# Kernel optimization log

Hardware: AMD Instinct MI355X
Metric: run time of the kernel (lower is better)

The kernel has to match this reference:

```python
import jax, jax.numpy as jnp
import numpy as np

ALPHA = 0.2  # leaky_relu negative slope
N = 100000
E = 3200000

def _gat_layer(h_in, edge, W, a):
    # h = x @ W ; score_e = leaky_relu([h_src || h_dst] @ a) computed without
    # materializing the [E, 2d] concat: a = [a_src; a_dst]
    h = h_in @ W                                  # [N, d]
    d = W.shape[1]
    s_src = h @ a[:d, 0]                          # [N]
    s_dst = h @ a[d:, 0]                          # [N]
    src, dst = edge[0], edge[1]
    score = jax.nn.leaky_relu(s_src[src] + s_dst[dst], negative_slope=ALPHA)  # [E]
    # sparse softmax over dim=1: normalize per source row (edge[0])
    m = jax.ops.segment_max(score, src, num_segments=N)      # [N], -inf for empty rows (never gathered)
    e = jnp.exp(score - m[src])                               # [E]
    z = jax.ops.segment_sum(e, src, num_segments=N)           # [N]
    attn = e / z[src]                                         # [E]
    # output[i] = sum_{(i,j) in E} attn_ij * h[j]; empty rows -> 0 (matches to_dense @ h)
    out = jax.ops.segment_sum(attn[:, None] * h[dst], src, num_segments=N)  # [N, d]
    return jax.nn.elu(out)

def setup_inputs() -> dict:
    key = jax.random.key(0)
    ks = jax.random.split(key, 8)
    return {
        "x": jax.random.normal(ks[0], (N, 256), dtype=jnp.float32),
        "edge": jax.random.randint(ks[1], (2, E), 0, N, dtype=jnp.int64) if jax.config.jax_enable_x64 else jax.random.randint(ks[1], (2, E), 0, N, dtype=jnp.int32),
        "W0": jax.random.normal(ks[2], (256, 256), dtype=jnp.float32) * 0.06,
        "a0": jax.random.normal(ks[3], (512, 1), dtype=jnp.float32) * 0.06,
        "W1": jax.random.normal(ks[4], (256, 128), dtype=jnp.float32) * 0.07,
        "a1": jax.random.normal(ks[5], (256, 1), dtype=jnp.float32) * 0.08,
        "lin_w": jax.random.normal(ks[6], (128, 40), dtype=jnp.float32) * 0.09,
        "lin_b": jax.random.normal(ks[7], (40,), dtype=jnp.float32) * 0.01,
    }

def reference(x, edge, W0, a0, W1, a1, lin_w, lin_b):
    # inference mode: dropout is identity
    h0 = _gat_layer(x, edge, W0, a0)    # [N, 256]
    h1 = _gat_layer(h0, edge, W1, a1)   # [N, 128]
    logits = h1 @ lin_w + lin_b         # [N, 40]
    return jax.nn.log_softmax(logits, axis=1)
```

## Files before the change

### kernel.cpp

```cpp
#include <hip/hip_runtime.h>
#include <cstddef>
#include <cstdint>

#define LRELU_ALPHA 0.2f
#define BIN_SHIFT 9
#define BIN_ROWS  (1 << BIN_SHIFT)
#define DST_BITS 17
#define DST_MASK ((1 << DST_BITS) - 1)

typedef _Float16 f16x8 __attribute__((ext_vector_type(8)));
typedef _Float16 f16x4 __attribute__((ext_vector_type(4)));
typedef _Float16 f16x2 __attribute__((ext_vector_type(2)));
typedef float    f32x4 __attribute__((ext_vector_type(4)));

__global__ __launch_bounds__(256) void bucket_count_kernel(const int* __restrict__ src,
                                                           int* __restrict__ bhist, int E)
{
    __shared__ int hist[256];
    int t = threadIdx.x;
    hist[t] = 0;
    __syncthreads();
    int base = blockIdx.x * 4096;
#pragma unroll
    for (int j = 0; j < 16; ++j) {
        int i = base + j * 256 + t;
        if (i < E) atomicAdd(&hist[src[i] >> BIN_SHIFT], 1);
    }
    __syncthreads();
    if (hist[t]) atomicAdd(&bhist[t], hist[t]);
}

__global__ __launch_bounds__(256) void bucket_scan_kernel(const int* __restrict__ bhist,
                                                          int* __restrict__ bbase,
                                                          int* __restrict__ gcur, int E)
{
    __shared__ int buf[256];
    int t = threadIdx.x;
    int v = bhist[t];
    buf[t] = v;
    __syncthreads();
    for (int off = 1; off < 256; off <<= 1) {
        int u = (t >= off) ? buf[t - off] : 0;
        __syncthreads();
        buf[t] += u;
        __syncthreads();
    }
    int excl = buf[t] - v;
    bbase[t] = excl;
    gcur[t] = excl;
    if (t == 255) bbase[256] = buf[255];
}

__global__ __launch_bounds__(256) void pass1_bin_kernel(const int* __restrict__ src,
                                                        const int* __restrict__ dst,
                                                        int* __restrict__ gcur,
                                                        int* __restrict__ pairs, int E)
{
    __shared__ int hist[256];
    __shared__ int cur[256];
    int t = threadIdx.x;
    hist[t] = 0;
    __syncthreads();
    int base = blockIdx.x * 4096;
    int s_[16], d_[16];
#pragma unroll
    for (int j = 0; j < 16; ++j) {
        int i = base + j * 256 + t;
        if (i < E) {
            s_[j] = src[i];
            d_[j] = dst[i];
            atomicAdd(&hist[s_[j] >> BIN_SHIFT], 1);
        } else s_[j] = -1;
    }
    __syncthreads();
    cur[t] = atomicAdd(&gcur[t], hist[t]);
    __syncthreads();
#pragma unroll
    for (int j = 0; j < 16; ++j) {
        if (s_[j] >= 0) {
            int pos = atomicAdd(&cur[s_[j] >> BIN_SHIFT], 1);
            pairs[pos] = ((s_[j] & (BIN_ROWS - 1)) << DST_BITS) | d_[j];
        }
    }
}

__global__ __launch_bounds__(256) void row_count_kernel(const int* __restrict__ pairs,
                                                        const int* __restrict__ bbase,
                                                        int* __restrict__ cnt, int N)
{
    __shared__ int c[BIN_ROWS];
    int b = blockIdx.x, t = threadIdx.x;
    int rowbase = b << BIN_SHIFT;
    int nrows = min(BIN_ROWS, N - rowbase);
    c[t] = 0; c[t + 256] = 0;
    __syncthreads();
    int beg = bbase[b], end = bbase[b + 1];
    for (int i = beg + t; i < end; i += 256)
        atomicAdd(&c[pairs[i] >> DST_BITS], 1);
    __syncthreads();
    if (t < nrows) cnt[rowbase + t] = c[t];
    if (t + 256 < nrows) cnt[rowbase + t + 256] = c[t + 256];
}

__global__ __launch_bounds__(256) void bsum_kernel(const int* __restrict__ cnt,
                                                   int* __restrict__ bsum, int n)
{
    __shared__ int red[4];
    int b = blockIdx.x, t = threadIdx.x;
    int base = b * 1024;
    int s = 0;
#pragma unroll
    for (int j = 0; j < 4; ++j) {
        int i = base + j * 256 + t;
        s += (i < n) ? cnt[i] : 0;
    }
#pragma unroll
    for (int off = 32; off; off >>= 1) s += __shfl_xor(s, off);
    if ((t & 63) == 0) red[t >> 6] = s;
    __syncthreads();
    if (t == 0) bsum[b] = red[0] + red[1] + red[2] + red[3];
}

__global__ __launch_bounds__(128) void bscan_kernel(int* __restrict__ bsum, int nb,
                                                    int* __restrict__ rowptr, int N)
{
    __shared__ int buf[128];
    int t = threadIdx.x;
    int v = (t < nb) ? bsum[t] : 0;
    buf[t] = v;
    __syncthreads();
    for (int off = 1; off < 128; off <<= 1) {
        int u = (t >= off) ? buf[t - off] : 0;
        __syncthreads();
        buf[t] += u;
        __syncthreads();
    }
    if (t < nb) bsum[t] = buf[t] - v;
    if (t == 127) rowptr[N] = buf[127];
}

__global__ __launch_bounds__(256) void chunkscan_kernel(const int* __restrict__ cnt,
                                                        const int* __restrict__ bsum,
                                                        int* __restrict__ rowptr, int n)
{
    __shared__ int tsum[256];
    int b = blockIdx.x, t = threadIdx.x;
    int base = b * 1024 + t * 4;
    int c[4];
    int s = 0;
#pragma unroll
    for (int j = 0; j < 4; ++j) {
        int i = base + j;
        c[j] = (i < n) ? cnt[i] : 0;
        s += c[j];
    }
    tsum[t] = s;
    __syncthreads();
    for (int off = 1; off < 256; off <<= 1) {
        int u = (t >= off) ? tsum[t - off] : 0;
        __syncthreads();
        tsum[t] += u;
        __syncthreads();
    }
    int run = bsum[b] + tsum[t] - s;
#pragma unroll
    for (int j = 0; j < 4; ++j) {
        int i = base + j;
        if (i < n) { rowptr[i] = run; run += c[j]; }
    }
}

__global__ __launch_bounds__(256) void pass2_scatter_kernel(const int* __restrict__ pairs,
                                                            const int* __restrict__ bbase,
                                                            const int* __restrict__ rowptr,
                                                            int* __restrict__ csr_dst, int N)
{
    __shared__ int cur[BIN_ROWS];
    int b = blockIdx.x, t = threadIdx.x;
    int rowbase = b << BIN_SHIFT;
    int nrows = min(BIN_ROWS, N - rowbase);
    if (t < nrows) cur[t] = rowptr[rowbase + t];
    if (t + 256 < nrows) cur[t + 256] = rowptr[rowbase + t + 256];
    __syncthreads();
    int beg = bbase[b], end = bbase[b + 1];
    for (int i = beg + t; i < end; i += 256) {
        int p = pairs[i];
        int pos = atomicAdd(&cur[p >> DST_BITS], 1);
        csr_dst[pos] = p & DST_MASK;
    }
}

__global__ __launch_bounds__(256) void transpose16_kernel(const float* __restrict__ W,
                                                          _Float16* __restrict__ Wt,
                                                          int K, int Nw)
{
    int i = blockIdx.x * 256 + threadIdx.x;
    if (i < K * Nw) {
        int n = i / K, k = i - n * K;
        Wt[i] = (_Float16)W[(size_t)k * Nw + n];
    }
}

#define GBM 64
#define GBK 32
#define LDP 40

template <bool CVTA, bool FUSE_S, int GBN>
__global__ __launch_bounds__(256) void gemm16_kernel(const void* __restrict__ Ap,
                                                     const _Float16* __restrict__ Bt,
                                                     _Float16* __restrict__ C,
                                                     int M, int K,
                                                     const float* __restrict__ avec,
                                                     int aoff,
                                                     float* __restrict__ ssrc,
                                                     float* __restrict__ sdst)
{
    constexpr int NT = GBN / 64;
    __shared__ __align__(16) _Float16 Ash[GBM * LDP];
    __shared__ __align__(16) _Float16 Bsh[GBN * LDP];
    const int tid = threadIdx.x;
    const int lane = tid & 63;
    const int w = tid >> 6;
    const int m0 = blockIdx.x * GBM;
    const int l15 = lane & 15;
    const int kq = lane >> 4;
    const int sr = tid >> 2;
    const int sc = tid & 3;
    const int wc = w * (GBN / 4);

    f32x4 acc[4][NT] = {};

    for (int k0 = 0; k0 < K; k0 += GBK) {
        {
            int gm = m0 + sr;
            f16x8 v = {};
            if (gm < M) {
                if constexpr (CVTA) {
                    const float* Af = (const float*)Ap;
                    float4 u0 = *(const float4*)(Af + (size_t)gm * K + k0 + sc * 8);
                    float4 u1 = *(const float4*)(Af + (size_t)gm * K + k0 + sc * 8 + 4);
                    v[0] = (_Float16)u0.x; v[1] = (_Float16)u0.y;
                    v[2] = (_Float16)u0.z; v[3] = (_Float16)u0.w;
                    v[4] = (_Float16)u1.x; v[5] = (_Float16)u1.y;
                    v[6] = (_Float16)u1.z; v[7] = (_Float16)u1.w;
                } else {
                    v = *(const f16x8*)((const _Float16*)Ap + (size_t)gm * K + k0 + sc * 8);
                }
            }
            *(f16x8*)&Ash[sr * LDP + sc * 8] = v;
        }
#pragma unroll
        for (int it = 0; it < GBN / 64; ++it) {
            int r = sr + it * 64;
            f16x8 v = *(const f16x8*)(Bt + (size_t)r * K + k0 + sc * 8);
            *(f16x8*)&Bsh[r * LDP + sc * 8] = v;
        }
        __syncthreads();

        f16x8 af[4], bf[NT];
#pragma unroll
        for (int mt = 0; mt < 4; ++mt)
            af[mt] = *(const f16x8*)&Ash[(mt * 16 + l15) * LDP + kq * 8];
#pragma unroll
        for (int nt = 0; nt < NT; ++nt)
            bf[nt] = *(const f16x8*)&Bsh[(wc + nt * 16 + l15) * LDP + kq * 8];
#pragma unroll
        for (int mt = 0; mt < 4; ++mt)
#pragma unroll
            for (int nt = 0; nt < NT; ++nt)
                acc[mt][nt] = __builtin_amdgcn_mfma_f32_16x16x32_f16(af[mt], bf[nt],
                                                                     acc[mt][nt], 0, 0, 0);
        __syncthreads();
    }

#pragma unroll
    for (int mt = 0; mt < 4; ++mt) {
#pragma unroll
        for (int r = 0; r < 4; ++r) {
            int gm = m0 + mt * 16 + kq * 4 + r;
            if (gm < M) {
#pragma unroll
                for (int nt = 0; nt < NT; ++nt)
                    C[(size_t)gm * GBN + wc + nt * 16 + l15] = (_Float16)acc[mt][nt][r];
            }
        }
    }

    if constexpr (FUSE_S) {
        float as[NT], ad[NT];
#pragma unroll
        for (int nt = 0; nt < NT; ++nt) {
            int c = wc + nt * 16 + l15;
            as[nt] = avec[c];
            ad[nt] = avec[aoff + c];
        }
#pragma unroll
        for (int mt = 0; mt < 4; ++mt) {
#pragma unroll
            for (int r = 0; r < 4; ++r) {
                float ps = 0.f, pd = 0.f;
#pragma unroll
                for (int nt = 0; nt < NT; ++nt) {
                    float v = acc[mt][nt][r];
                    ps += v * as[nt];
                    pd += v * ad[nt];
                }
#pragma unroll
                for (int off = 1; off < 16; off <<= 1) {
                    ps += __shfl_xor(ps, off);
                    pd += __shfl_xor(pd, off);
                }
                int gm = m0 + mt * 16 + kq * 4 + r;
                if (l15 == 0 && gm < M) {
                    atomicAdd(&ssrc[gm], ps);
                    atomicAdd(&sdst[gm], pd);
                }
            }
        }
    }
}

__device__ __forceinline__ float eluf(float x) { return x > 0.f ? x : expm1f(x); }

union h2u { f16x2 h; unsigned u; };
__device__ __forceinline__ unsigned pkadd(unsigned a, unsigned b)
{
    h2u x, y; x.u = a; y.u = b; x.h += y.h; return x.u;
}

template <int D>
__global__ __launch_bounds__(256) void attnagg_kernel(const _Float16* __restrict__ h,
                                                      const float* __restrict__ ssrc,
                                                      const float* __restrict__ sdst,
                                                      const int* __restrict__ csr_dst,
                                                      const int* __restrict__ rowptr,
                                                      float* __restrict__ attn_spill,
                                                      _Float16* __restrict__ out, int nrows)
{
    constexpr int HPL = D / 16;
    constexpr int NV = HPL / 8;
    __shared__ float2 wdbuf[4][128];
    int lane = threadIdx.x & 63;
    int wv = threadIdx.x >> 6;
    int row = blockIdx.x * 4 + wv;
    if (row >= nrows) return;
    int beg = rowptr[row], end = rowptr[row + 1];
    int deg = end - beg;
    bool small = (deg <= 128);

    if (deg > 0) {
        float ss = ssrc[row];
        if (small) {
            int e0 = beg + lane, e1 = e0 + 64;
            int d0 = 0, d1 = 0;
            float sc0 = -INFINITY, sc1 = -INFINITY;
            if (e0 < end) {
                d0 = csr_dst[e0];
                float sc = ss + sdst[d0];
                sc0 = (sc > 0.f) ? sc : LRELU_ALPHA * sc;
            }
            if (e1 < end) {
                d1 = csr_dst[e1];
                float sc = ss + sdst[d1];
                sc1 = (sc > 0.f) ? sc : LRELU_ALPHA * sc;
            }
            float m = fmaxf(sc0, sc1);
#pragma unroll
            for (int off = 32; off; off >>= 1) m = fmaxf(m, __shfl_xor(m, off));
            float ex0 = (e0 < end) ? expf(sc0 - m) : 0.f;
            float ex1 = (e1 < end) ? expf(sc1 - m) : 0.f;
            float z = ex0 + ex1;
#pragma unroll
            for (int off = 32; off; off >>= 1) z += __shfl_xor(z, off);
            float rz = 1.f / z;
            if (e0 < end) wdbuf[wv][lane] = make_float2(ex0 * rz, __int_as_float(d0));
            if (e1 < end) wdbuf[wv][64 + lane] = make_float2(ex1 * rz, __int_as_float(d1));
        } else {
            float m = -INFINITY;
            for (int e = beg + lane; e < end; e += 64) {
                float sc = ss + sdst[csr_dst[e]];
                sc = (sc > 0.f) ? sc : LRELU_ALPHA * sc;
                attn_spill[e] = sc;
                m = fmaxf(m, sc);
            }
#pragma unroll
            for (int off = 32; off; off >>= 1) m = fmaxf(m, __shfl_xor(m, off));
            float z = 0.f;
            for (int e = beg + lane; e < end; e += 64) {
                float ex = expf(attn_spill[e] - m);
                attn_spill[e] = ex;
                z += ex;
            }
#pragma unroll
            for (int off = 32; off; off >>= 1) z += __shfl_xor(z, off);
            float rz = 1.f / z;
            for (int e = beg + lane; e < end; e += 64) attn_spill[e] *= rz;
        }
    }

    int sub = lane >> 4;
    int cl = lane & 15;
    const _Float16* hbase = h + cl * HPL;
    f16x8 acc[NV] = {};

    if (small) {
        int k = sub;
        for (; k + 12 < deg; k += 16) {
            float2 wd0 = wdbuf[wv][k];
            float2 wd1 = wdbuf[wv][k + 4];
            float2 wd2 = wdbuf[wv][k + 8];
            float2 wd3 = wdbuf[wv][k + 12];
            const _Float16* p0 = hbase + ((unsigned)__float_as_int(wd0.y) * D);
            const _Float16* p1 = hbase + ((unsigned)__float_as_int(wd1.y) * D);
            const _Float16* p2 = hbase + ((unsigned)__float_as_int(wd2.y) * D);
            const _Float16* p3 = hbase + ((unsigned)__float_as_int(wd3.y) * D);
            f16x8 v0[NV], v1[NV], v2[NV], v3[NV];
#pragma unroll
            for (int q = 0; q < NV; ++q) v0[q] = *(const f16x8*)(p0 + q * 8);
#pragma unroll
            for (int q = 0; q < NV; ++q) v1[q] = *(const f16x8*)(p1 + q * 8);
#pragma unroll
            for (int q = 0; q < NV; ++q) v2[q] = *(const f16x8*)(p2 + q * 8);
#pragma unroll
            for (int q = 0; q < NV; ++q) v3[q] = *(const f16x8*)(p3 + q * 8);
            _Float16 w0 = (_Float16)wd0.x, w1 = (_Float16)wd1.x;
            _Float16 w2 = (_Float16)wd2.x, w3 = (_Float16)wd3.x;
            f16x8 a0 = {w0, w0, w0, w0, w0, w0, w0, w0};
            f16x8 a1 = {w1, w1, w1, w1, w1, w1, w1, w1};
            f16x8 a2 = {w2, w2, w2, w2, w2, w2, w2, w2};
            f16x8 a3 = {w3, w3, w3, w3, w3, w3, w3, w3};
#pragma unroll
            for (int q = 0; q < NV; ++q) acc[q] += v0[q] * a0;
#pragma unroll
            for (int q = 0; q < NV; ++q) acc[q] += v1[q] * a1;
#pragma unroll
            for (int q = 0; q < NV; ++q) acc[q] += v2[q] * a2;
#pragma unroll
            for (int q = 0; q < NV; ++q) acc[q] += v3[q] * a3;
        }
        for (; k < deg; k += 4) {
            float2 wd = wdbuf[wv][k];
            const _Float16* hp = hbase + ((unsigned)__float_as_int(wd.y) * D);
            f16x8 vv[NV];
#pragma unroll
            for (int q = 0; q < NV; ++q) vv[q] = *(const f16x8*)(hp + q * 8);
            _Float16 wh = (_Float16)wd.x;
            f16x8 a8 = {wh, wh, wh, wh, wh, wh, wh, wh};
#pragma unroll
            for (int q = 0; q < NV; ++q) acc[q] += vv[q] * a8;
        }
    } else {
        for (int k = sub; k < deg; k += 4) {
            float a = attn_spill[beg + k];
            int d = csr_dst[beg + k];
            const _Float16* hp = hbase + ((unsigned)d * D);
            f16x8 vv[NV];
#pragma unroll
            for (int q = 0; q < NV; ++q) vv[q] = *(const f16x8*)(hp + q * 8);
            _Float16 wh = (_Float16)a;
            f16x8 a8 = {wh, wh, wh, wh, wh, wh, wh, wh};
#pragma unroll
            for (int q = 0; q < NV; ++q) acc[q] += vv[q] * a8;
        }
    }

    union { f16x8 v; unsigned w[4]; } A[NV];
#pragma unroll
    for (int q = 0; q < NV; ++q) A[q].v = acc[q];
#pragma unroll
    for (int q = 0; q < NV; ++q)
#pragma unroll
        for (int i = 0; i < 4; ++i) {
            unsigned u = A[q].w[i];
            u = pkadd(u, (unsigned)__shfl_xor((int)u, 16));
            u = pkadd(u, (unsigned)__shfl_xor((int)u, 32));
            A[q].w[i] = u;
        }
    if (sub == 0) {
        _Float16* op = out + (size_t)row * D + cl * HPL;
#pragma unroll
        for (int q = 0; q < NV; ++q) {
            f16x8 o;
#pragma unroll
            for (int j = 0; j < 8; ++j) o[j] = (_Float16)eluf((float)A[q].v[j]);
            *(f16x8*)(op + q * 8) = o;
        }
    }
}

__global__ __launch_bounds__(256) void final16_kernel(const _Float16* __restrict__ h,
                                                      const float* __restrict__ lw,
                                                      const float* __restrict__ lb,
                                                      float* __restrict__ out, int nrows)
{
    __shared__ __align__(16) float rowbuf[4][128];
    int lane = threadIdx.x & 63;
    int wv = threadIdx.x >> 6;
    int row = blockIdx.x * 4 + wv;
    bool active = row < nrows;
    if (active) {
        f16x2 v = *(const f16x2*)&h[(size_t)row * 128 + lane * 2];
        rowbuf[wv][lane * 2] = (float)v[0];
        rowbuf[wv][lane * 2 + 1] = (float)v[1];
    }
    __syncthreads();
    float logit = 0.f;
    if (active && lane < 40) {
        float s = lb[lane];
        for (int k = 0; k < 128; ++k) s += rowbuf[wv][k] * lw[k * 40 + lane];
        logit = s;
    }
    float v = (active && lane < 40) ? logit : -INFINITY;
#pragma unroll
    for (int off = 32; off; off >>= 1) v = fmaxf(v, __shfl_xor(v, off));
    float ex = (active && lane < 40) ? expf(logit - v) : 0.f;
    float zs = ex;
#pragma unroll
    for (int off = 32; off; off >>= 1) zs += __shfl_xor(zs, off);
    if (active && lane < 40) out[(size_t)row * 40 + lane] = logit - v - logf(zs);
}

extern "C" void kernel_launch(void* const* d_in, const int* in_sizes, int n_in,
                              void* d_out, int out_size, void* d_ws, size_t ws_size,
                              hipStream_t stream)
{
    const float* x   = (const float*)d_in[0];
    const int*  edge = (const int*)d_in[1];
    const float* W0  = (const float*)d_in[2];
    const float* a0  = (const float*)d_in[3];
    const float* W1  = (const float*)d_in[4];
    const float* a1  = (const float*)d_in[5];
    const float* lw  = (const float*)d_in[6];
    const float* lb  = (const float*)d_in[7];
    float* out = (float*)d_out;

    const int N = in_sizes[0] / 256;
    const int E = in_sizes[1] / 2;
    const int* src = edge;
    const int* dst = edge + E;

    _Float16* bufA = (_Float16*)d_ws;
    _Float16* bufB = bufA + (size_t)N * 256;
    _Float16* W0t  = bufB + (size_t)N * 256;
    _Float16* W1t  = W0t + 256 * 256;
    float* ssrc = (float*)(W1t + 128 * 256);
    float* sdst = ssrc + N;
    float* attn = sdst + N;
    int* rowptr  = (int*)(attn + E);
    int* cnt     = rowptr + (N + 1);
    int* csr_dst = cnt + N;
    int* bsum    = csr_dst + E;
    int* bhist   = bsum + 128;
    int* bbase   = bhist + 256;
    int* gcur    = bbase + 257;
    int* pairs   = (int*)bufA;

    const int rowBlocks = (N + 3) / 4;
    const int nb = (N + 1023) / 1024;
    const int NB = (N + BIN_ROWS - 1) >> BIN_SHIFT;
    const int blocksE = (E + 4095) / 4096;
    const int gemmBlocks = (N + GBM - 1) / GBM;

    hipMemsetAsync(bhist, 0, 256 * sizeof(int), stream);
    bucket_count_kernel<<<blocksE, 256, 0, stream>>>(src, bhist, E);
    bucket_scan_kernel<<<1, 256, 0, stream>>>(bhist, bbase, gcur, E);
    pass1_bin_kernel<<<blocksE, 256, 0, stream>>>(src, dst, gcur, pairs, E);
    row_count_kernel<<<NB, 256, 0, stream>>>(pairs, bbase, cnt, N);
    bsum_kernel<<<nb, 256, 0, stream>>>(cnt, bsum, N);
    bscan_kernel<<<1, 128, 0, stream>>>(bsum, nb, rowptr, N);
    chunkscan_kernel<<<nb, 256, 0, stream>>>(cnt, bsum, rowptr, N);
    pass2_scatter_kernel<<<NB, 256, 0, stream>>>(pairs, bbase, rowptr, csr_dst, N);

    transpose16_kernel<<<(256 * 256 + 255) / 256, 256, 0, stream>>>(W0, W0t, 256, 256);
    transpose16_kernel<<<(128 * 256 + 255) / 256, 256, 0, stream>>>(W1, W1t, 256, 128);

    hipMemsetAsync(ssrc, 0, (size_t)2 * N * sizeof(float), stream);
    gemm16_kernel<true, true, 256><<<gemmBlocks, 256, 0, stream>>>(
        x, W0t, bufA, N, 256, a0, 256, ssrc, sdst);
    attnagg_kernel<256><<<rowBlocks, 256, 0, stream>>>(bufA, ssrc, sdst, csr_dst, rowptr, attn, bufB, N);

    hipMemsetAsync(ssrc, 0, (size_t)2 * N * sizeof(float), stream);
    gemm16_kernel<false, true, 128><<<gemmBlocks, 256, 0, stream>>>(
        bufB, W1t, bufA, N, 256, a1, 128, ssrc, sdst);
    attnagg_kernel<128><<<rowBlocks, 256, 0, stream>>>(bufA, ssrc, sdst, csr_dst, rowptr, attn, bufB, N);

    final16_kernel<<<rowBlocks, 256, 0, stream>>>(bufB, lw, lb, out, N);
}
```

Baseline: 647.6 us.

## Fuse prep and scan kernels, double-buffer GEMM, fold final linear into attention

Merges the weight transposes and histogram clear into one prep kernel. Replaces the three-kernel row-pointer scan with a per-bin scan seeded by bin offsets. Double-buffers the GEMM shared tiles so global loads overlap MFMA work. Reduces the attention-score partials in shared memory instead of using global atomics, which also removes the memsets. Fuses the final linear layer and log-softmax into the second attention kernel. The aim is fewer launches and less memory traffic, at the cost of more shared memory and register pressure in the GEMM.

New measurement: 616.3 us. 1.05x faster.

```diff
diff --git a/kernel.cpp b/kernel.cpp
--- a/kernel.cpp
+++ b/kernel.cpp
@@ -12,6 +12,25 @@
 typedef _Float16 f16x4 __attribute__((ext_vector_type(4)));
 typedef _Float16 f16x2 __attribute__((ext_vector_type(2)));
 typedef float    f32x4 __attribute__((ext_vector_type(4)));
+
+__global__ __launch_bounds__(256) void prep_kernel(const float* __restrict__ W0,
+                                                   const float* __restrict__ W1,
+                                                   _Float16* __restrict__ W0t,
+                                                   _Float16* __restrict__ W1t,
+                                                   int* __restrict__ bhist)
+{
+    int i = blockIdx.x * 256 + threadIdx.x;
+    if (i < 65536) {
+        int n = i >> 8, k = i & 255;
+        W0t[i] = (_Float16)W0[k * 256 + n];
+    } else if (i < 98304) {
+        int j = i - 65536;
+        int n = j >> 8, k = j & 255;
+        W1t[j] = (_Float16)W1[k * 128 + n];
+    } else if (i < 98304 + 256) {
+        bhist[i - 98304] = 0;
+    }
+}
 
 __global__ __launch_bounds__(256) void bucket_count_kernel(const int* __restrict__ src,
                                                            int* __restrict__ bhist, int E)
@@ -84,11 +103,13 @@
     }
 }
 
-__global__ __launch_bounds__(256) void row_count_kernel(const int* __restrict__ pairs,
-                                                        const int* __restrict__ bbase,
-                                                        int* __restrict__ cnt, int N)
+__global__ __launch_bounds__(256) void rowptr_kernel(const int* __restrict__ pairs,
+                                                     const int* __restrict__ bbase,
+                                                     int* __restrict__ rowptr,
+                                                     int N, int E)
 {
     __shared__ int c[BIN_ROWS];
+    __shared__ int tsum[256];
     int b = blockIdx.x, t = threadIdx.x;
     int rowbase = b << BIN_SHIFT;
     int nrows = min(BIN_ROWS, N - rowbase);
@@ -98,62 +119,8 @@
     for (int i = beg + t; i < end; i += 256)
         atomicAdd(&c[pairs[i] >> DST_BITS], 1);
     __syncthreads();
-    if (t < nrows) cnt[rowbase + t] = c[t];
-    if (t + 256 < nrows) cnt[rowbase + t + 256] = c[t + 256];
-}
-
-__global__ __launch_bounds__(256) void bsum_kernel(const int* __restrict__ cnt,
-                                                   int* __restrict__ bsum, int n)
-{
-    __shared__ int red[4];
-    int b = blockIdx.x, t = threadIdx.x;
-    int base = b * 1024;
-    int s = 0;
-#pragma unroll
-    for (int j = 0; j < 4; ++j) {
-        int i = base + j * 256 + t;
-        s += (i < n) ? cnt[i] : 0;
-    }
-#pragma unroll
-    for (int off = 32; off; off >>= 1) s += __shfl_xor(s, off);
-    if ((t & 63) == 0) red[t >> 6] = s;
-    __syncthreads();
-    if (t == 0) bsum[b] = red[0] + red[1] + red[2] + red[3];
-}
-
-__global__ __launch_bounds__(128) void bscan_kernel(int* __restrict__ bsum, int nb,
-                                                    int* __restrict__ rowptr, int N)
-{
-    __shared__ int buf[128];
-    int t = threadIdx.x;
-    int v = (t < nb) ? bsum[t] : 0;
-    buf[t] = v;
-    __syncthreads();
-    for (int off = 1; off < 128; off <<= 1) {
-        int u = (t >= off) ? buf[t - off] : 0;
-        __syncthreads();
-        buf[t] += u;
-        __syncthreads();
-    }
-    if (t < nb) bsum[t] = buf[t] - v;
-    if (t == 127) rowptr[N] = buf[127];
-}
-
-__global__ __launch_bounds__(256) void chunkscan_kernel(const int* __restrict__ cnt,
-                                                        const int* __restrict__ bsum,
-                                                        int* __restrict__ rowptr, int n)
-{
-    __shared__ int tsum[256];
-    int b = blockIdx.x, t = threadIdx.x;
-    int base = b * 1024 + t * 4;
-    int c[4];
-    int s = 0;
-#pragma unroll
-    for (int j = 0; j < 4; ++j) {
-        int i = base + j;
-        c[j] = (i < n) ? cnt[i] : 0;
-        s += c[j];
-    }
+    int c0 = c[2 * t], c1 = c[2 * t + 1];
+    int s = c0 + c1;
     tsum[t] = s;
     __syncthreads();
     for (int off = 1; off < 256; off <<= 1) {
@@ -162,12 +129,10 @@
         tsum[t] += u;
         __syncthreads();
     }
-    int run = bsum[b] + tsum[t] - s;
-#pragma unroll
-    for (int j = 0; j < 4; ++j) {
-        int i = base + j;
-        if (i < n) { rowptr[i] = run; run += c[j]; }
-    }
+    int excl = beg + tsum[t] - s;
+    if (2 * t < nrows)     rowptr[rowbase + 2 * t] = excl;
+    if (2 * t + 1 < nrows) rowptr[rowbase + 2 * t + 1] = excl + c0;
+    if (b == (int)gridDim.x - 1 && t == 0) rowptr[N] = E;
 }
 
 __global__ __launch_bounds__(256) void pass2_scatter_kernel(const int* __restrict__ pairs,
@@ -187,17 +152,6 @@
         int p = pairs[i];
         int pos = atomicAdd(&cur[p >> DST_BITS], 1);
         csr_dst[pos] = p & DST_MASK;
-    }
-}
-
-__global__ __launch_bounds__(256) void transpose16_kernel(const float* __restrict__ W,
-                                                          _Float16* __restrict__ Wt,
-                                                          int K, int Nw)
-{
-    int i = blockIdx.x * 256 + threadIdx.x;
-    if (i < K * Nw) {
-        int n = i / K, k = i - n * K;
-        Wt[i] = (_Float16)W[(size_t)k * Nw + n];
     }
 }
 
@@ -216,8 +170,9 @@
                                                      float* __restrict__ sdst)
 {
     constexpr int NT = GBN / 64;
-    __shared__ __align__(16) _Float16 Ash[GBM * LDP];
-    __shared__ __align__(16) _Float16 Bsh[GBN * LDP];
+    __shared__ __align__(16) _Float16 Ash[2][GBM * LDP];
+    __shared__ __align__(16) _Float16 Bsh[2][GBN * LDP];
+    __shared__ float2 spart[4][GBM];
     const int tid = threadIdx.x;
     const int lane = tid & 63;
     const int w = tid >> 6;
@@ -227,50 +182,62 @@
     const int sr = tid >> 2;
     const int sc = tid & 3;
     const int wc = w * (GBN / 4);
+    const int gmS = m0 + sr;
+
+    f16x8 va, vb[NT];
+    auto loadT = [&](int k0, f16x8& a, f16x8* b) {
+        a = f16x8{};
+        if (gmS < M) {
+            if constexpr (CVTA) {
+                const float* Af = (const float*)Ap;
+                float4 u0 = *(const float4*)(Af + (size_t)gmS * K + k0 + sc * 8);
+                float4 u1 = *(const float4*)(Af + (size_t)gmS * K + k0 + sc * 8 + 4);
+                a[0] = (_Float16)u0.x; a[1] = (_Float16)u0.y;
+                a[2] = (_Float16)u0.z; a[3] = (_Float16)u0.w;
+                a[4] = (_Float16)u1.x; a[5] = (_Float16)u1.y;
+                a[6] = (_Float16)u1.z; a[7] = (_Float16)u1.w;
+            } else {
+                a = *(const f16x8*)((const _Float16*)Ap + (size_t)gmS * K + k0 + sc * 8);
+            }
+        }
+#pragma unroll
+        for (int it = 0; it < NT; ++it)
+            b[it] = *(const f16x8*)(Bt + (size_t)(sr + it * 64) * K + k0 + sc * 8);
+    };
+    auto storeT = [&](int buf, const f16x8& a, const f16x8* b) {
+        *(f16x8*)&Ash[buf][sr * LDP + sc * 8] = a;
+#pragma unroll
+        for (int it = 0; it < NT; ++it)
+            *(f16x8*)&Bsh[buf][(sr + it * 64) * LDP + sc * 8] = b[it];
+    };
+
+    loadT(0, va, vb);
+    storeT(0, va, vb);
+    __syncthreads();
 
     f32x4 acc[4][NT] = {};
-
+    int cur = 0;
     for (int k0 = 0; k0 < K; k0 += GBK) {
-        {
-            int gm = m0 + sr;
-            f16x8 v = {};
-            if (gm < M) {
-                if constexpr (CVTA) {
-                    const float* Af = (const float*)Ap;
-                    float4 u0 = *(const float4*)(Af + (size_t)gm * K + k0 + sc * 8);
-                    float4 u1 = *(const float4*)(Af + (size_t)gm * K + k0 + sc * 8 + 4);
-                    v[0] = (_Float16)u0.x; v[1] = (_Float16)u0.y;
-                    v[2] = (_Float16)u0.z; v[3] = (_Float16)u0.w;
-                    v[4] = (_Float16)u1.x; v[5] = (_Float16)u1.y;
-                    v[6] = (_Float16)u1.z; v[7] = (_Float16)u1.w;
-                } else {
-                    v = *(const f16x8*)((const _Float16*)Ap + (size_t)gm * K + k0 + sc * 8);
-                }
-            }
-            *(f16x8*)&Ash[sr * LDP + sc * 8] = v;
-        }
-#pragma unroll
-        for (int it = 0; it < GBN / 64; ++it) {
-            int r = sr + it * 64;
-            f16x8 v = *(const f16x8*)(Bt + (size_t)r * K + k0 + sc * 8);
-            *(f16x8*)&Bsh[r * LDP + sc * 8] = v;
-        }
-        __syncthreads();
+        bool nxt = (k0 + GBK) < K;
+        f16x8 na, nb[NT];
+        if (nxt) loadT(k0 + GBK, na, nb);
 
         f16x8 af[4], bf[NT];
 #pragma unroll
         for (int mt = 0; mt < 4; ++mt)
-            af[mt] = *(const f16x8*)&Ash[(mt * 16 + l15) * LDP + kq * 8];
+            af[mt] = *(const f16x8*)&Ash[cur][(mt * 16 + l15) * LDP + kq * 8];
 #pragma unroll
         for (int nt = 0; nt < NT; ++nt)
-            bf[nt] = *(const f16x8*)&Bsh[(wc + nt * 16 + l15) * LDP + kq * 8];
+            bf[nt] = *(const f16x8*)&Bsh[cur][(wc + nt * 16 + l15) * LDP + kq * 8];
 #pragma unroll
         for (int mt = 0; mt < 4; ++mt)
 #pragma unroll
             for (int nt = 0; nt < NT; ++nt)
                 acc[mt][nt] = __builtin_amdgcn_mfma_f32_16x16x32_f16(af[mt], bf[nt],
                                                                      acc[mt][nt], 0, 0, 0);
+        if (nxt) storeT(cur ^ 1, na, nb);
         __syncthreads();
+        cur ^= 1;
     }
 
 #pragma unroll
@@ -310,11 +277,18 @@
                     ps += __shfl_xor(ps, off);
                     pd += __shfl_xor(pd, off);
                 }
-                int gm = m0 + mt * 16 + kq * 4 + r;
-                if (l15 == 0 && gm < M) {
-                    atomicAdd(&ssrc[gm], ps);
-                    atomicAdd(&sdst[gm], pd);
-                }
+                int lr = mt * 16 + kq * 4 + r;
+                if (l15 == 0) spart[w][lr] = make_float2(ps, pd);
+            }
+        }
+        __syncthreads();
+        if (tid < GBM) {
+            float2 p0 = spart[0][tid], p1 = spart[1][tid];
+            float2 p2 = spart[2][tid], p3 = spart[3][tid];
+            int gm = m0 + tid;
+            if (gm < M) {
+                ssrc[gm] = p0.x + p1.x + p2.x + p3.x;
+                sdst[gm] = p0.y + p1.y + p2.y + p3.y;
             }
         }
     }
@@ -328,18 +302,22 @@
     h2u x, y; x.u = a; y.u = b; x.h += y.h; return x.u;
 }
 
-template <int D>
+template <int D, bool FUSE_FINAL>
 __global__ __launch_bounds__(256) void attnagg_kernel(const _Float16* __restrict__ h,
                                                       const float* __restrict__ ssrc,
                                                       const float* __restrict__ sdst,
                                                       const int* __restrict__ csr_dst,
                                                       const int* __restrict__ rowptr,
                                                       float* __restrict__ attn_spill,
-                                                      _Float16* __restrict__ out, int nrows)
+                                                      _Float16* __restrict__ out16,
+                                                      const float* __restrict__ lw,
+                                                      const float* __restrict__ lb,
+                                                      float* __restrict__ outf, int nrows)
 {
     constexpr int HPL = D / 16;
     constexpr int NV = HPL / 8;
     __shared__ float2 wdbuf[4][128];
+    __shared__ float rowbuf[FUSE_FINAL ? 4 : 1][128];
     int lane = threadIdx.x & 63;
     int wv = threadIdx.x >> 6;
     int row = blockIdx.x * 4 + wv;
@@ -476,48 +454,41 @@
             u = pkadd(u, (unsigned)__shfl_xor((int)u, 32));
             A[q].w[i] = u;
         }
-    if (sub == 0) {
-        _Float16* op = out + (size_t)row * D + cl * HPL;
-#pragma unroll
-        for (int q = 0; q < NV; ++q) {
-            f16x8 o;
-#pragma unroll
-            for (int j = 0; j < 8; ++j) o[j] = (_Float16)eluf((float)A[q].v[j]);
-            *(f16x8*)(op + q * 8) = o;
-        }
-    }
-}
-
-__global__ __launch_bounds__(256) void final16_kernel(const _Float16* __restrict__ h,
-                                                      const float* __restrict__ lw,
-                                                      const float* __restrict__ lb,
-                                                      float* __restrict__ out, int nrows)
-{
-    __shared__ __align__(16) float rowbuf[4][128];
-    int lane = threadIdx.x & 63;
-    int wv = threadIdx.x >> 6;
-    int row = blockIdx.x * 4 + wv;
-    bool active = row < nrows;
-    if (active) {
-        f16x2 v = *(const f16x2*)&h[(size_t)row * 128 + lane * 2];
-        rowbuf[wv][lane * 2] = (float)v[0];
-        rowbuf[wv][lane * 2 + 1] = (float)v[1];
-    }
-    __syncthreads();
-    float logit = 0.f;
-    if (active && lane < 40) {
-        float s = lb[lane];
-        for (int k = 0; k < 128; ++k) s += rowbuf[wv][k] * lw[k * 40 + lane];
-        logit = s;
-    }
-    float v = (active && lane < 40) ? logit : -INFINITY;
-#pragma unroll
-    for (int off = 32; off; off >>= 1) v = fmaxf(v, __shfl_xor(v, off));
-    float ex = (active && lane < 40) ? expf(logit - v) : 0.f;
-    float zs = ex;
-#pragma unroll
-    for (int off = 32; off; off >>= 1) zs += __shfl_xor(zs, off);
-    if (active && lane < 40) out[(size_t)row * 40 + lane] = logit - v - logf(zs);
+
+    if constexpr (!FUSE_FINAL) {
+        if (sub == 0) {
+            _Float16* op = out16 + (size_t)row * D + cl * HPL;
+#pragma unroll
+            for (int q = 0; q < NV; ++q) {
+                f16x8 o;
+#pragma unroll
+                for (int j = 0; j < 8; ++j) o[j] = (_Float16)eluf((float)A[q].v[j]);
+                *(f16x8*)(op + q * 8) = o;
+            }
+        }
+    } else {
+        if (sub == 0) {
+#pragma unroll
+            for (int j = 0; j < 8; ++j)
+                rowbuf[wv][cl * 8 + j] = eluf((float)A[0].v[j]);
+        }
+        __builtin_amdgcn_wave_barrier();
+        float logit = 0.f;
+        if (lane < 40) {
+            float s = lb[lane];
+#pragma unroll 4
+            for (int k = 0; k < 128; ++k) s += rowbuf[wv][k] * lw[k * 40 + lane];
+            logit = s;
+        }
+        float v = (lane < 40) ? logit : -INFINITY;
+#pragma unroll
+        for (int off = 32; off; off >>= 1) v = fmaxf(v, __shfl_xor(v, off));
+        float ex = (lane < 40) ? expf(logit - v) : 0.f;
+        float zs = ex;
+#pragma unroll
+        for (int off = 32; off; off >>= 1) zs += __shfl_xor(zs, off);
+        if (lane < 40) outf[(size_t)row * 40 + lane] = logit - v - logf(zs);
+    }
 }
 
 extern "C" void kernel_launch(void* const* d_in, const int* in_sizes, int n_in,
@@ -547,42 +518,32 @@
     float* sdst = ssrc + N;
     float* attn = sdst + N;
     int* rowptr  = (int*)(attn + E);
-    int* cnt     = rowptr + (N + 1);
-    int* csr_dst = cnt + N;
-    int* bsum    = csr_dst + E;
-    int* bhist   = bsum + 128;
+    int* csr_dst = rowptr + (N + 1);
+    int* bhist   = csr_dst + E;
     int* bbase   = bhist + 256;
     int* gcur    = bbase + 257;
     int* pairs   = (int*)bufA;
 
     const int rowBlocks = (N + 3) / 4;
-    const int nb = (N + 1023) / 1024;
     const int NB = (N + BIN_ROWS - 1) >> BIN_SHIFT;
     const int blocksE = (E + 4095) / 4096;
     const int gemmBlocks = (N + GBM - 1) / GBM;
 
-    hipMemsetAsync(bhist, 0, 256 * sizeof(int), stream);
+    prep_kernel<<<385, 256, 0, stream>>>(W0, W1, W0t, W1t, bhist);
+
     bucket_count_kernel<<<blocksE, 256, 0, stream>>>(src, bhist, E);
     bucket_scan_kernel<<<1, 256, 0, stream>>>(bhist, bbase, gcur, E);
     pass1_bin_kernel<<<blocksE, 256, 0, stream>>>(src, dst, gcur, pairs, E);
-    row_count_kernel<<<NB, 256, 0, stream>>>(pairs, bbase, cnt, N);
-    bsum_kernel<<<nb, 256, 0, stream>>>(cnt, bsum, N);
-    bscan_kernel<<<1, 128, 0, stream>>>(bsum, nb, rowptr, N);
-    chunkscan_kernel<<<nb, 256, 0, stream>>>(cnt, bsum, rowptr, N);
+    rowptr_kernel<<<NB, 256, 0, stream>>>(pairs, bbase, rowptr, N, E);
     pass2_scatter_kernel<<<NB, 256, 0, stream>>>(pairs, bbase, rowptr, csr_dst, N);
 
-    transpose16_kernel<<<(256 * 256 + 255) / 256, 256, 0, stream>>>(W0, W0t, 256, 256);
-    transpose16_kernel<<<(128 * 256 + 255) / 256, 256, 0, stream>>>(W1, W1t, 256, 128);
-
-    hipMemsetAsync(ssrc, 0, (size_t)2 * N * sizeof(float), stream);
     gemm16_kernel<true, true, 256><<<gemmBlocks, 256, 0, stream>>>(
         x, W0t, bufA, N, 256, a0, 256, ssrc, sdst);
-    attnagg_kernel<256><<<rowBlocks, 256, 0, stream>>>(bufA, ssrc, sdst, csr_dst, rowptr, attn, bufB, N);
-
-    hipMemsetAsync(ssrc, 0, (size_t)2 * N * sizeof(float), stream);
+    attnagg_kernel<256, false><<<rowBlocks, 256, 0, stream>>>(
+        bufA, ssrc, sdst, csr_dst, rowptr, attn, bufB, nullptr, nullptr, nullptr, N);
+
     gemm16_kernel<false, true, 128><<<gemmBlocks, 256, 0, stream>>>(
         bufB, W1t, bufA, N, 256, a1, 128, ssrc, sdst);
-    attnagg_kernel<128><<<rowBlocks, 256, 0, stream>>>(bufA, ssrc, sdst, csr_dst, rowptr, attn, bufB, N);
-
-    final16_kernel<<<rowBlocks, 256, 0, stream>>>(bufB, lw, lb, out, N);
-}
+    attnagg_kernel<128, true><<<rowBlocks, 256, 0, stream>>>(
+        bufA, ssrc, sdst, csr_dst, rowptr, attn, nullptr, lw, lb, out, N);
+}
```
